# Kernel tuning notes

Measured on AMD Instinct MI355X. Metric: run time of the kernel, lower is better.

The kernel has to match this reference:

```python
import jax, jax.numpy as jnp
import numpy as np

# Dims: N batch, C=in=out channels, T frames, V joints, S subsets, R rel_channels, H SE hidden
N, C, T, V = 256, 64, 64, 25
S, R = 3, C // 8           # num_subset, rel_channels = in_channels // rel_reduction
O = C                       # out_channels
H = max(4, O // 4)          # SE attention_channels
BN_EPS = 1e-5


def setup_inputs() -> dict:
    key = jax.random.key(0)
    ks = jax.random.split(key, 12)
    sc = 0.1
    return {
        "x":     jax.random.normal(ks[0], (N, C, T, V), jnp.float32),
        "PA":    jax.random.normal(ks[1], (S, V, V), jnp.float32) * sc,
        "alpha": jnp.ones((S,), jnp.float32),
        # per-subset stacked 1x1-conv weights (kernel_size=1 -> plain matrices)
        "w1": jax.random.normal(ks[2], (S, R, C), jnp.float32) * (2.0 / C) ** 0.5,
        "b1": jnp.zeros((S, R), jnp.float32),
        "w2": jax.random.normal(ks[3], (S, R, C), jnp.float32) * (2.0 / C) ** 0.5,
        "b2": jnp.zeros((S, R), jnp.float32),
        "w3": jax.random.normal(ks[4], (S, O, C), jnp.float32) * (2.0 / C) ** 0.5,
        "b3": jnp.zeros((S, O), jnp.float32),
        "w4": jax.random.normal(ks[5], (S, O, R), jnp.float32) * (2.0 / R) ** 0.5,
        "b4": jnp.zeros((S, O), jnp.float32),
        # final BN (eval mode: running_mean=0, running_var=1)
        "bn_w": jnp.ones((O,), jnp.float32),
        "bn_b": jnp.zeros((O,), jnp.float32),
        # SE channel attention
        "se_w1": jax.random.normal(ks[6], (H, O), jnp.float32) * (2.0 / O) ** 0.5,
        "se_b1": jnp.zeros((H,), jnp.float32),
        "se_w2": jax.random.normal(ks[7], (O, H), jnp.float32) * (2.0 / H) ** 0.5,
        "se_b2": jnp.zeros((O,), jnp.float32),
    }


def reference(x, PA, alpha, w1, b1, w2, b2, w3, b3, w4, b4,
              bn_w, bn_b, se_w1, se_b1, se_w2, se_b2):
    # --- CTRGC for all S subsets at once ---
    # conv1(x).mean(-2) == conv1 applied to x.mean over T (1x1 conv is linear)
    xm = x.mean(axis=2)                                            # [N,C,V]
    x1 = jnp.einsum('ncv,src->nsrv', xm, w1) + b1[None, :, :, None]
    x2 = jnp.einsum('ncv,src->nsrv', xm, w2) + b2[None, :, :, None]
    x3 = jnp.einsum('nctv,soc->nsotv', x, w3) + b3[None, :, :, None, None]
    # outer-difference + tanh attention map: [N,S,R,V(u),V(v)]
    att = jnp.tanh(x1[..., :, None] - x2[..., None, :])
    m = jnp.einsum('nsruv,sor->nsouv', att, w4) + b4[None, :, :, None, None]
    Asym = PA + jnp.swapaxes(PA, -1, -2)                           # A + A^T, [S,V,V]
    m = m * alpha[None, :, None, None, None] + Asym[None, :, None, :, :]
    m = jax.nn.softmax(m, axis=-2)                                 # softmax over u (dim=-2)
    # einsum 'ncuv,nctv->nctu' per subset, summed over subsets
    y = jnp.einsum('nsouv,nsotv->notu', m, x3)                     # [N,O,T,V]
    # --- BatchNorm2d (eval: mean 0, var 1) ---
    y = y / jnp.sqrt(1.0 + BN_EPS) * bn_w[None, :, None, None] + bn_b[None, :, None, None]
    # --- SE channel attention ---
    pooled = y.mean(axis=(2, 3))                                   # [N,O]
    h = jax.nn.relu(pooled @ se_w1.T + se_b1)
    se = jax.nn.sigmoid(h @ se_w2.T + se_b2)
    y = y * se[:, :, None, None]
    # --- residual (in==out -> identity down) + ReLU ---
    return jax.nn.relu(y + x)
```

## Files before the change

### kernel.cpp

```cpp
#include <hip/hip_runtime.h>

#define NN 256
#define CC 64
#define TT 64
#define VV 25
#define SS 3
#define RR 8
#define OO 64
#define HH 16

typedef _Float16 f16;
typedef _Float16 f16x8 __attribute__((ext_vector_type(8)));
typedef float f32x4 __attribute__((ext_vector_type(4)));

#define IBN 0.9999950000374997f

#define MG_NSTRIDE 153600

__device__ __forceinline__ float tanh_fast(float xx) {
  float e = __expf(2.0f * xx);
  return 1.0f - __fdividef(2.0f, e + 1.0f);
}

__global__ __launch_bounds__(256) void k1(
    const float* __restrict__ x, const float* __restrict__ PA,
    const float* __restrict__ alpha,
    const float* __restrict__ w1, const float* __restrict__ b1,
    const float* __restrict__ w2, const float* __restrict__ b2,
    const float* __restrict__ w3, const float* __restrict__ b3,
    const float* __restrict__ w4, const float* __restrict__ b4,
    const float* __restrict__ bn_w, const float* __restrict__ bn_b,
    const float* __restrict__ se_w1, const float* __restrict__ se_b1,
    const float* __restrict__ se_w2, const float* __restrict__ se_b2,
    f16* __restrict__ m_g, float* __restrict__ se_g, f16* __restrict__ w3p_g)
{
  __shared__ float part[64][4][25];
  __shared__ float xms[1600];
  __shared__ float x1s[600], x2s[600];
  __shared__ float w1s[1536], w2s[1536];
  __shared__ float asym_s[1875];
  __shared__ __attribute__((aligned(16))) float att2[5000];
  __shared__ __attribute__((aligned(16))) f16 mt[16][25][32];
  __shared__ float xmv[64], pooledv[64], hbuf[16];

  int n = blockIdx.x, tid = threadIdx.x;

  for (int i = tid; i < 1536; i += 256) { w1s[i] = w1[i]; w2s[i] = w2[i]; }
  for (int i = tid; i < 1875; i += 256) {
    int s = i / 625, rem = i - s*625, u = rem / 25, v = rem - u*25;
    asym_s[i] = PA[s*625 + u*25 + v] + PA[s*625 + v*25 + u];
  }
  for (int i = tid; i < 2800; i += 256) {
    int o = i / 175, rem = i - o*175, u = rem / 7, k = rem - u*7;
    mt[o][u][25 + k] = (f16)0.f;
  }

  {
    int c = tid >> 2, tq = tid & 3;
    const float* p = x + (size_t)(n*64 + c)*1600 + tq*400;
    float acc[25];
    #pragma unroll
    for (int i = 0; i < 25; ++i) acc[i] = 0.f;
    for (int blk = 0; blk < 4; ++blk) {
      const float* pb = p + blk*100;
      #pragma unroll
      for (int j = 0; j < 25; ++j) {
        f32x4 vv = *(const f32x4*)(pb + 4*j);
        acc[(4*j + 0) % 25] += vv[0];
        acc[(4*j + 1) % 25] += vv[1];
        acc[(4*j + 2) % 25] += vv[2];
        acc[(4*j + 3) % 25] += vv[3];
      }
    }
    #pragma unroll
    for (int i = 0; i < 25; ++i) part[c][tq][i] = acc[i];
  }
  __syncthreads();

  for (int idx = tid; idx < 1600; idx += 256) {
    int cc = idx / 25, v = idx - cc*25;
    xms[idx] = (part[cc][0][v] + part[cc][1][v] + part[cc][2][v] + part[cc][3][v])
               * (1.0f/64.0f);
  }
  __syncthreads();

  for (int idx = tid; idx < 600; idx += 256) {
    int sr = idx / 25, v = idx - sr*25;
    float a1 = b1[sr], a2 = b2[sr];
    #pragma unroll
    for (int c = 0; c < 64; ++c) {
      float xv = xms[c*25 + v];
      a1 += xv * w1s[sr*64 + c];
      a2 += xv * w2s[sr*64 + c];
    }
    x1s[idx] = a1; x2s[idx] = a2;
  }

  if (tid < 64) {
    float s = 0.f;
    #pragma unroll
    for (int v = 0; v < 25; ++v) s += xms[tid*25 + v];
    xmv[tid] = s * (1.0f/25.0f);
  }
  __syncthreads();
  if (tid < 64) {
    int o = tid;
    float pp = b3[o] + b3[64 + o] + b3[128 + o];
    for (int cc = 0; cc < 64; ++cc)
      pp += xmv[cc] * (w3[o*64 + cc] + w3[4096 + o*64 + cc] + w3[8192 + o*64 + cc]);
    pooledv[o] = IBN * bn_w[o] * pp + bn_b[o];
  }
  __syncthreads();
  if (tid < 16) {
    float hh = se_b1[tid];
    for (int o = 0; o < 64; ++o) hh += pooledv[o] * se_w1[tid*64 + o];
    hbuf[tid] = fmaxf(hh, 0.0f);
  }
  __syncthreads();
  if (tid < 64) {
    float t = se_b2[tid];
    for (int j = 0; j < 16; ++j) t += hbuf[j] * se_w2[tid*16 + j];
    se_g[n*64 + tid] = 1.0f / (1.0f + __expf(-t));
  }

  f16x8* mg8 = (f16x8*)(m_g + (size_t)n*MG_NSTRIDE);
  for (int s = 0; s < 3; ++s) {
    __syncthreads();
    for (int idx = tid; idx < 5000; idx += 256) {
      int uv = idx >> 3, r = idx & 7;
      int u = uv / 25, v = uv - u*25;
      att2[idx] = tanh_fast(x1s[(s*8 + r)*25 + u] - x2s[(s*8 + r)*25 + v]);
    }
    __syncthreads();

    float alphav = alpha[s];
    for (int oq = 0; oq < 4; ++oq) {
      if (tid < 200) {
        int ot = tid / 25, v = tid - ot*25;
        int o0 = oq*16 + ot*2;
        float w4r[2][8], b4r[2];
        #pragma unroll
        for (int oo = 0; oo < 2; ++oo) {
          b4r[oo] = b4[s*64 + o0 + oo];
          #pragma unroll
          for (int r = 0; r < 8; ++r) w4r[oo][r] = w4[(s*64 + o0 + oo)*8 + r];
        }
        float acc[2][25];
        #pragma unroll
        for (int u = 0; u < 25; ++u) {
          const float* ap = &att2[(u*25 + v)*8];
          f32x4 a0 = *(const f32x4*)ap;
          f32x4 a1 = *(const f32x4*)(ap + 4);
          float asv = asym_s[s*625 + u*25 + v];
          #pragma unroll
          for (int oo = 0; oo < 2; ++oo) {
            float t = b4r[oo];
            t += a0[0]*w4r[oo][0] + a0[1]*w4r[oo][1] + a0[2]*w4r[oo][2] + a0[3]*w4r[oo][3];
            t += a1[0]*w4r[oo][4] + a1[1]*w4r[oo][5] + a1[2]*w4r[oo][6] + a1[3]*w4r[oo][7];
            acc[oo][u] = t*alphav + asv;
          }
        }
        #pragma unroll
        for (int oo = 0; oo < 2; ++oo) {
          float mx = -1e30f;
          #pragma unroll
          for (int u = 0; u < 25; ++u) mx = fmaxf(mx, acc[oo][u]);
          float sum = 0.f;
          #pragma unroll
          for (int u = 0; u < 25; ++u) {
            float e = __expf(acc[oo][u] - mx); acc[oo][u] = e; sum += e;
          }
          float inv = 1.0f / sum;
          #pragma unroll
          for (int u = 0; u < 25; ++u) mt[ot*2 + oo][u][v] = (f16)(acc[oo][u]*inv);
        }
      }
      __syncthreads();
      for (int idx = tid; idx < 1600; idx += 256) {
        int ol = idx / 100, rem = idx - ol*100, u = rem >> 2, vc = rem & 3;
        int o = oq*16 + ol;
        mg8[((size_t)(s*64 + o)*25 + u)*4 + vc] = *(const f16x8*)&mt[ol][u][vc*8];
      }
      __syncthreads();
    }
  }

  if (n == 0) {
    for (int idx = tid; idx < 12288; idx += 256) {
      int j = idx & 7, lane = (idx >> 3) & 63, kk = (idx >> 9) & 1, mi = idx >> 10;
      int s = mi >> 2, o = ((mi & 3) << 4) + (lane & 15);
      int cc = kk*32 + ((lane >> 4) << 3) + j;
      w3p_g[idx] = (f16)w3[(s*64 + o)*64 + cc];
    }
  }
}

struct __align__(16) SmemC {
  f16   xsT[400][72];
  f16   zs[16][16][40];
  float b3s[192];
};

__global__ __launch_bounds__(256, 2) void kc(
    const float* __restrict__ x, const float* __restrict__ b3,
    const float* __restrict__ bn_w, const float* __restrict__ bn_b,
    const f16* __restrict__ m_g, const float* __restrict__ se_g,
    const f16* __restrict__ w3p_g, float* __restrict__ out)
{
  __shared__ SmemC sm;
  int bid = blockIdx.x;
  int xcd = bid & 7, ii = bid >> 3;
  int n = xcd*32 + (ii >> 2), tt = ii & 3;
  int tid = threadIdx.x;
  int lane = tid & 63, w = tid >> 6, q = lane >> 4, l15 = lane & 15;

  {
    const float* xb = x + (size_t)n*CC*1600 + tt*400;
    #pragma unroll
    for (int it = 0; it < 50; ++it) {
      int idx = it*256 + tid;
      int cp = idx / 400, j = idx - cp*400;
      float v0 = xb[(2*cp)*1600 + j];
      float v1 = xb[(2*cp + 1)*1600 + j];
      f16* p = &sm.xsT[j][2*cp];
      p[0] = (f16)v0; p[1] = (f16)v1;
    }
    if (tid < 192) sm.b3s[tid] = b3[tid];
    for (int i = tid; i < 3840; i += 256) {
      int op = i / 240, rem = i - op*240, t = rem / 15, v = 25 + (rem - t*15);
      sm.zs[op][t][v] = (f16)0.f;
    }
  }
  __syncthreads();

  const f16x8* w3pv = (const f16x8*)w3p_g;
  const f16x8* mgv  = (const f16x8*)(m_g + (size_t)n*MG_NSTRIDE);

  for (int ob = 0; ob < 4; ++ob) {
    f32x4 yacc[4][2];
    #pragma unroll
    for (int i = 0; i < 4; ++i) {
      yacc[i][0] = (f32x4){0.f,0.f,0.f,0.f};
      yacc[i][1] = (f32x4){0.f,0.f,0.f,0.f};
    }

    for (int s = 0; s < 3; ++s) {
      f16x8 bm[4][2];
      int u2 = 16 + l15; if (u2 > 24) u2 = 24;
      #pragma unroll
      for (int i = 0; i < 4; ++i) {
        int o = ob*16 + w*4 + i;
        int rb = (s*64 + o)*25;
        bm[i][0] = mgv[(rb + l15)*4 + q];
        bm[i][1] = mgv[(rb + u2)*4 + q];
      }
      int mi = s*4 + ob;
      f16x8 a0 = w3pv[(mi*2 + 0)*64 + lane];
      f16x8 a1 = w3pv[(mi*2 + 1)*64 + lane];

      __syncthreads();

      for (int ni = w; ni < 25; ni += 4) {
        int row = ni*16 + l15;
        f16x8 bf0 = *(const f16x8*)&sm.xsT[row][q*8];
        f16x8 bf1 = *(const f16x8*)&sm.xsT[row][32 + q*8];
        f32x4 acc = (f32x4){0.f,0.f,0.f,0.f};
        acc = __builtin_amdgcn_mfma_f32_16x16x32_f16(a0, bf0, acc, 0, 0, 0);
        acc = __builtin_amdgcn_mfma_f32_16x16x32_f16(a1, bf1, acc, 0, 0, 0);
        int t = row / 25, v = row - t*25;
        #pragma unroll
        for (int rg = 0; rg < 4; ++rg) {
          int op = q*4 + rg;
          sm.zs[op][t][v] = (f16)(acc[rg] + sm.b3s[s*64 + ob*16 + op]);
        }
      }
      __syncthreads();

      #pragma unroll
      for (int i = 0; i < 4; ++i) {
        int op = w*4 + i;
        f16x8 az = *(const f16x8*)&sm.zs[op][l15][q*8];
        yacc[i][0] = __builtin_amdgcn_mfma_f32_16x16x32_f16(az, bm[i][0], yacc[i][0], 0, 0, 0);
        yacc[i][1] = __builtin_amdgcn_mfma_f32_16x16x32_f16(az, bm[i][1], yacc[i][1], 0, 0, 0);
      }
    }

    #pragma unroll
    for (int i = 0; i < 4; ++i) {
      int op = w*4 + i, o = ob*16 + op;
      float sev   = se_g[n*64 + o];
      float scale = IBN * bn_w[o] * sev;
      float bias  = bn_b[o] * sev;
      #pragma unroll
      for (int ut = 0; ut < 2; ++ut) {
        int u = ut*16 + l15;
        if (u < 25) {
          #pragma unroll
          for (int rg = 0; rg < 4; ++rg) {
            int t = q*4 + rg;
            float xres = (float)sm.xsT[t*25 + u][o];
            float val = yacc[i][ut][rg]*scale + bias + xres;
            out[(((size_t)n*64 + o)*64 + tt*16 + t)*25 + u] = fmaxf(val, 0.0f);
          }
        }
      }
    }
  }
}

extern "C" void kernel_launch(void* const* d_in, const int* in_sizes, int n_in,
                              void* d_out, int out_size, void* d_ws, size_t ws_size,
                              hipStream_t stream)
{
  const float* x    = (const float*)d_in[0];
  const float* PA   = (const float*)d_in[1];
  const float* alp  = (const float*)d_in[2];
  const float* w1   = (const float*)d_in[3];
  const float* b1   = (const float*)d_in[4];
  const float* w2   = (const float*)d_in[5];
  const float* b2   = (const float*)d_in[6];
  const float* w3   = (const float*)d_in[7];
  const float* b3   = (const float*)d_in[8];
  const float* w4   = (const float*)d_in[9];
  const float* b4   = (const float*)d_in[10];
  const float* bnw  = (const float*)d_in[11];
  const float* bnb  = (const float*)d_in[12];
  const float* sw1  = (const float*)d_in[13];
  const float* sb1  = (const float*)d_in[14];
  const float* sw2  = (const float*)d_in[15];
  const float* sb2  = (const float*)d_in[16];

  char* ws = (char*)d_ws;
  f16*   m_g   = (f16*)ws;
  float* se_g  = (float*)(ws + 78643200);
  f16*   w3p_g = (f16*)(ws + 78643200 + 65536);

  float* out = (float*)d_out;

  k1<<<256, 256, 0, stream>>>(x, PA, alp, w1, b1, w2, b2, w3, b3, w4, b4,
                              bnw, bnb, sw1, sb1, sw2, sb2, m_g, se_g, w3p_g);
  kc<<<1024, 256, 0, stream>>>(x, b3, bnw, bnb, m_g, se_g, w3p_g, out);
}
```

Baseline: 363.3 us.

## Widen both kernels to 512 threads and restructure work split per block

k1 now runs 512 threads per block. The mean reduction, the softmax map work and the m staging are split across twice as many threads, and the staging buffer gets an XOR-swizzled layout to reduce LDS bank conflicts. kc now uses 512 blocks of 512 threads, and each block processes two T-quarters sequentially. The x tile load is rewritten to pack 8 channels into a single vector LDS store, and each wave handles 2 output channels instead of 4. The aim is better occupancy and latency hiding in k1, which only launches 256 blocks, but kc gets half as many blocks and more synchronisation points per block.

Measured after the change: 327.6 us. 9.8% less time.

```diff
diff --git a/kernel.cpp b/kernel.cpp
--- a/kernel.cpp
+++ b/kernel.cpp
@@ -22,7 +22,11 @@
   return 1.0f - __fdividef(2.0f, e + 1.0f);
 }
 
-__global__ __launch_bounds__(256) void k1(
+__device__ __forceinline__ int mti(int mo, int u, int v) {
+  return (mo*800 + u*32 + v) ^ ((mo & 6) << 2);
+}
+
+__global__ __launch_bounds__(512) void k1(
     const float* __restrict__ x, const float* __restrict__ PA,
     const float* __restrict__ alpha,
     const float* __restrict__ w1, const float* __restrict__ b1,
@@ -34,34 +38,34 @@
     const float* __restrict__ se_w2, const float* __restrict__ se_b2,
     f16* __restrict__ m_g, float* __restrict__ se_g, f16* __restrict__ w3p_g)
 {
-  __shared__ float part[64][4][25];
+  __shared__ float part[64][8][25];
   __shared__ float xms[1600];
   __shared__ float x1s[600], x2s[600];
   __shared__ float w1s[1536], w2s[1536];
   __shared__ float asym_s[1875];
   __shared__ __attribute__((aligned(16))) float att2[5000];
-  __shared__ __attribute__((aligned(16))) f16 mt[16][25][32];
+  __shared__ __attribute__((aligned(16))) f16 mtf[25600];
   __shared__ float xmv[64], pooledv[64], hbuf[16];
 
   int n = blockIdx.x, tid = threadIdx.x;
 
-  for (int i = tid; i < 1536; i += 256) { w1s[i] = w1[i]; w2s[i] = w2[i]; }
-  for (int i = tid; i < 1875; i += 256) {
+  for (int i = tid; i < 1536; i += 512) { w1s[i] = w1[i]; w2s[i] = w2[i]; }
+  for (int i = tid; i < 1875; i += 512) {
     int s = i / 625, rem = i - s*625, u = rem / 25, v = rem - u*25;
     asym_s[i] = PA[s*625 + u*25 + v] + PA[s*625 + v*25 + u];
   }
-  for (int i = tid; i < 2800; i += 256) {
-    int o = i / 175, rem = i - o*175, u = rem / 7, k = rem - u*7;
-    mt[o][u][25 + k] = (f16)0.f;
+  for (int i = tid; i < 5600; i += 512) {
+    int mo = i / 175, rem = i - mo*175, u = rem / 7, v = 25 + (rem - u*7);
+    mtf[mti(mo, u, v)] = (f16)0.f;
   }
 
   {
-    int c = tid >> 2, tq = tid & 3;
-    const float* p = x + (size_t)(n*64 + c)*1600 + tq*400;
+    int c = tid >> 3, tq = tid & 7;
+    const float* p = x + (size_t)(n*64 + c)*1600 + tq*200;
     float acc[25];
     #pragma unroll
     for (int i = 0; i < 25; ++i) acc[i] = 0.f;
-    for (int blk = 0; blk < 4; ++blk) {
+    for (int blk = 0; blk < 2; ++blk) {
       const float* pb = p + blk*100;
       #pragma unroll
       for (int j = 0; j < 25; ++j) {
@@ -77,14 +81,16 @@
   }
   __syncthreads();
 
-  for (int idx = tid; idx < 1600; idx += 256) {
+  for (int idx = tid; idx < 1600; idx += 512) {
     int cc = idx / 25, v = idx - cc*25;
-    xms[idx] = (part[cc][0][v] + part[cc][1][v] + part[cc][2][v] + part[cc][3][v])
-               * (1.0f/64.0f);
-  }
-  __syncthreads();
-
-  for (int idx = tid; idx < 600; idx += 256) {
+    float s = 0.f;
+    #pragma unroll
+    for (int tq = 0; tq < 8; ++tq) s += part[cc][tq][v];
+    xms[idx] = s * (1.0f/64.0f);
+  }
+  __syncthreads();
+
+  for (int idx = tid; idx < 600; idx += 512) {
     int sr = idx / 25, v = idx - sr*25;
     float a1 = b1[sr], a2 = b2[sr];
     #pragma unroll
@@ -126,7 +132,7 @@
   f16x8* mg8 = (f16x8*)(m_g + (size_t)n*MG_NSTRIDE);
   for (int s = 0; s < 3; ++s) {
     __syncthreads();
-    for (int idx = tid; idx < 5000; idx += 256) {
+    for (int idx = tid; idx < 5000; idx += 512) {
       int uv = idx >> 3, r = idx & 7;
       int u = uv / 25, v = uv - u*25;
       att2[idx] = tanh_fast(x1s[(s*8 + r)*25 + u] - x2s[(s*8 + r)*25 + v]);
@@ -134,10 +140,10 @@
     __syncthreads();
 
     float alphav = alpha[s];
-    for (int oq = 0; oq < 4; ++oq) {
-      if (tid < 200) {
+    for (int oh = 0; oh < 2; ++oh) {
+      if (tid < 400) {
         int ot = tid / 25, v = tid - ot*25;
-        int o0 = oq*16 + ot*2;
+        int o0 = oh*32 + ot*2;
         float w4r[2][8], b4r[2];
         #pragma unroll
         for (int oo = 0; oo < 2; ++oo) {
@@ -162,6 +168,7 @@
         }
         #pragma unroll
         for (int oo = 0; oo < 2; ++oo) {
+          int mo = ot*2 + oo;
           float mx = -1e30f;
           #pragma unroll
           for (int u = 0; u < 25; ++u) mx = fmaxf(mx, acc[oo][u]);
@@ -172,21 +179,22 @@
           }
           float inv = 1.0f / sum;
           #pragma unroll
-          for (int u = 0; u < 25; ++u) mt[ot*2 + oo][u][v] = (f16)(acc[oo][u]*inv);
+          for (int u = 0; u < 25; ++u) mtf[mti(mo, u, v)] = (f16)(acc[oo][u]*inv);
         }
       }
       __syncthreads();
-      for (int idx = tid; idx < 1600; idx += 256) {
-        int ol = idx / 100, rem = idx - ol*100, u = rem >> 2, vc = rem & 3;
-        int o = oq*16 + ol;
-        mg8[((size_t)(s*64 + o)*25 + u)*4 + vc] = *(const f16x8*)&mt[ol][u][vc*8];
+      for (int idx = tid; idx < 3200; idx += 512) {
+        int mo = idx / 100, rem = idx - mo*100, u = rem >> 2, vc = rem & 3;
+        int o = oh*32 + mo;
+        f16x8 val = *(const f16x8*)&mtf[mti(mo, u, vc*8)];
+        mg8[((size_t)(s*64 + o)*25 + u)*4 + vc] = val;
       }
       __syncthreads();
     }
   }
 
   if (n == 0) {
-    for (int idx = tid; idx < 12288; idx += 256) {
+    for (int idx = tid; idx < 12288; idx += 512) {
       int j = idx & 7, lane = (idx >> 3) & 63, kk = (idx >> 9) & 1, mi = idx >> 10;
       int s = mi >> 2, o = ((mi & 3) << 4) + (lane & 15);
       int cc = kk*32 + ((lane >> 4) << 3) + j;
@@ -201,7 +209,7 @@
   float b3s[192];
 };
 
-__global__ __launch_bounds__(256, 2) void kc(
+__global__ __launch_bounds__(512, 4) void kc(
     const float* __restrict__ x, const float* __restrict__ b3,
     const float* __restrict__ bn_w, const float* __restrict__ bn_b,
     const f16* __restrict__ m_g, const float* __restrict__ se_g,
@@ -210,97 +218,101 @@
   __shared__ SmemC sm;
   int bid = blockIdx.x;
   int xcd = bid & 7, ii = bid >> 3;
-  int n = xcd*32 + (ii >> 2), tt = ii & 3;
+  int n = xcd*32 + (ii >> 1), th = ii & 1;
   int tid = threadIdx.x;
   int lane = tid & 63, w = tid >> 6, q = lane >> 4, l15 = lane & 15;
 
-  {
-    const float* xb = x + (size_t)n*CC*1600 + tt*400;
-    #pragma unroll
-    for (int it = 0; it < 50; ++it) {
-      int idx = it*256 + tid;
-      int cp = idx / 400, j = idx - cp*400;
-      float v0 = xb[(2*cp)*1600 + j];
-      float v1 = xb[(2*cp + 1)*1600 + j];
-      f16* p = &sm.xsT[j][2*cp];
-      p[0] = (f16)v0; p[1] = (f16)v1;
-    }
-    if (tid < 192) sm.b3s[tid] = b3[tid];
-    for (int i = tid; i < 3840; i += 256) {
-      int op = i / 240, rem = i - op*240, t = rem / 15, v = 25 + (rem - t*15);
-      sm.zs[op][t][v] = (f16)0.f;
-    }
-  }
-  __syncthreads();
+  if (tid < 192) sm.b3s[tid] = b3[tid];
+  for (int i = tid; i < 3840; i += 512) {
+    int op = i / 240, rem = i - op*240, t = rem / 15, v = 25 + (rem - t*15);
+    sm.zs[op][t][v] = (f16)0.f;
+  }
 
   const f16x8* w3pv = (const f16x8*)w3p_g;
   const f16x8* mgv  = (const f16x8*)(m_g + (size_t)n*MG_NSTRIDE);
 
-  for (int ob = 0; ob < 4; ++ob) {
-    f32x4 yacc[4][2];
-    #pragma unroll
-    for (int i = 0; i < 4; ++i) {
-      yacc[i][0] = (f32x4){0.f,0.f,0.f,0.f};
-      yacc[i][1] = (f32x4){0.f,0.f,0.f,0.f};
-    }
-
-    for (int s = 0; s < 3; ++s) {
-      f16x8 bm[4][2];
-      int u2 = 16 + l15; if (u2 > 24) u2 = 24;
+  for (int tloc = 0; tloc < 2; ++tloc) {
+    int tt = th*2 + tloc;
+    __syncthreads();
+
+    {
+      const float* xb = x + (size_t)n*CC*1600 + tt*400;
+      for (int idx = tid; idx < 3200; idx += 512) {
+        int cb = idx / 400, j = idx - cb*400;
+        f16x8 hv;
+        #pragma unroll
+        for (int k = 0; k < 8; ++k) hv[k] = (f16)xb[(cb*8 + k)*1600 + j];
+        *(f16x8*)&sm.xsT[j][cb*8] = hv;
+      }
+    }
+    __syncthreads();
+
+    for (int ob = 0; ob < 4; ++ob) {
+      f32x4 yacc[2][2];
       #pragma unroll
-      for (int i = 0; i < 4; ++i) {
-        int o = ob*16 + w*4 + i;
-        int rb = (s*64 + o)*25;
-        bm[i][0] = mgv[(rb + l15)*4 + q];
-        bm[i][1] = mgv[(rb + u2)*4 + q];
-      }
-      int mi = s*4 + ob;
-      f16x8 a0 = w3pv[(mi*2 + 0)*64 + lane];
-      f16x8 a1 = w3pv[(mi*2 + 1)*64 + lane];
-
-      __syncthreads();
-
-      for (int ni = w; ni < 25; ni += 4) {
-        int row = ni*16 + l15;
-        f16x8 bf0 = *(const f16x8*)&sm.xsT[row][q*8];
-        f16x8 bf1 = *(const f16x8*)&sm.xsT[row][32 + q*8];
-        f32x4 acc = (f32x4){0.f,0.f,0.f,0.f};
-        acc = __builtin_amdgcn_mfma_f32_16x16x32_f16(a0, bf0, acc, 0, 0, 0);
-        acc = __builtin_amdgcn_mfma_f32_16x16x32_f16(a1, bf1, acc, 0, 0, 0);
-        int t = row / 25, v = row - t*25;
-        #pragma unroll
-        for (int rg = 0; rg < 4; ++rg) {
-          int op = q*4 + rg;
-          sm.zs[op][t][v] = (f16)(acc[rg] + sm.b3s[s*64 + ob*16 + op]);
-        }
-      }
-      __syncthreads();
+      for (int i = 0; i < 2; ++i) {
+        yacc[i][0] = (f32x4){0.f,0.f,0.f,0.f};
+        yacc[i][1] = (f32x4){0.f,0.f,0.f,0.f};
+      }
+
+      for (int s = 0; s < 3; ++s) {
+        f16x8 bm[2][2];
+        int u2 = 16 + l15; if (u2 > 24) u2 = 24;
+        #pragma unroll
+        for (int i = 0; i < 2; ++i) {
+          int o = ob*16 + w*2 + i;
+          int rb = (s*64 + o)*25;
+          bm[i][0] = mgv[(rb + l15)*4 + q];
+          bm[i][1] = mgv[(rb + u2)*4 + q];
+        }
+        int mi = s*4 + ob;
+        f16x8 a0 = w3pv[(mi*2 + 0)*64 + lane];
+        f16x8 a1 = w3pv[(mi*2 + 1)*64 + lane];
+
+        __syncthreads();
+
+        for (int ni = w; ni < 25; ni += 8) {
+          int row = ni*16 + l15;
+          f16x8 bf0 = *(const f16x8*)&sm.xsT[row][q*8];
+          f16x8 bf1 = *(const f16x8*)&sm.xsT[row][32 + q*8];
+          f32x4 acc = (f32x4){0.f,0.f,0.f,0.f};
+          acc = __builtin_amdgcn_mfma_f32_16x16x32_f16(a0, bf0, acc, 0, 0, 0);
+          acc = __builtin_amdgcn_mfma_f32_16x16x32_f16(a1, bf1, acc, 0, 0, 0);
+          int t = row / 25, v = row - t*25;
+          #pragma unroll
+          for (int rg = 0; rg < 4; ++rg) {
+            int op = q*4 + rg;
+            sm.zs[op][t][v] = (f16)(acc[rg] + sm.b3s[s*64 + ob*16 + op]);
+          }
+        }
+        __syncthreads();
+
+        #pragma unroll
+        for (int i = 0; i < 2; ++i) {
+          int op = w*2 + i;
+          f16x8 az = *(const f16x8*)&sm.zs[op][l15][q*8];
+          yacc[i][0] = __builtin_amdgcn_mfma_f32_16x16x32_f16(az, bm[i][0], yacc[i][0], 0, 0, 0);
+          yacc[i][1] = __builtin_amdgcn_mfma_f32_16x16x32_f16(az, bm[i][1], yacc[i][1], 0, 0, 0);
+        }
+      }
 
       #pragma unroll
-      for (int i = 0; i < 4; ++i) {
-        int op = w*4 + i;
-        f16x8 az = *(const f16x8*)&sm.zs[op][l15][q*8];
-        yacc[i][0] = __builtin_amdgcn_mfma_f32_16x16x32_f16(az, bm[i][0], yacc[i][0], 0, 0, 0);
-        yacc[i][1] = __builtin_amdgcn_mfma_f32_16x16x32_f16(az, bm[i][1], yacc[i][1], 0, 0, 0);
-      }
-    }
-
-    #pragma unroll
-    for (int i = 0; i < 4; ++i) {
-      int op = w*4 + i, o = ob*16 + op;
-      float sev   = se_g[n*64 + o];
-      float scale = IBN * bn_w[o] * sev;
-      float bias  = bn_b[o] * sev;
-      #pragma unroll
-      for (int ut = 0; ut < 2; ++ut) {
-        int u = ut*16 + l15;
-        if (u < 25) {
-          #pragma unroll
-          for (int rg = 0; rg < 4; ++rg) {
-            int t = q*4 + rg;
-            float xres = (float)sm.xsT[t*25 + u][o];
-            float val = yacc[i][ut][rg]*scale + bias + xres;
-            out[(((size_t)n*64 + o)*64 + tt*16 + t)*25 + u] = fmaxf(val, 0.0f);
+      for (int i = 0; i < 2; ++i) {
+        int op = w*2 + i, o = ob*16 + op;
+        float sev   = se_g[n*64 + o];
+        float scale = IBN * bn_w[o] * sev;
+        float bias  = bn_b[o] * sev;
+        #pragma unroll
+        for (int ut = 0; ut < 2; ++ut) {
+          int u = ut*16 + l15;
+          if (u < 25) {
+            #pragma unroll
+            for (int rg = 0; rg < 4; ++rg) {
+              int t = q*4 + rg;
+              float xres = (float)sm.xsT[t*25 + u][o];
+              float val = yacc[i][ut][rg]*scale + bias + xres;
+              out[(((size_t)n*64 + o)*64 + tt*16 + t)*25 + u] = fmaxf(val, 0.0f);
+            }
           }
         }
       }
@@ -337,7 +349,7 @@
 
   float* out = (float*)d_out;
 
-  k1<<<256, 256, 0, stream>>>(x, PA, alp, w1, b1, w2, b2, w3, b3, w4, b4,
+  k1<<<256, 512, 0, stream>>>(x, PA, alp, w1, b1, w2, b2, w3, b3, w4, b4,
                               bnw, bnb, sw1, sb1, sw2, sb2, m_g, se_g, w3p_g);
-  kc<<<1024, 256, 0, stream>>>(x, b3, bnw, bnb, m_g, se_g, w3p_g, out);
-}
+  kc<<<512, 512, 0, stream>>>(x, b3, bnw, bnb, m_g, se_g, w3p_g, out);
+}
```
